# Kernel optimization log

Hardware: AMD Instinct MI355X
Metric: run time of the kernel (lower is better)

Reference implementation:

```python
import jax, jax.numpy as jnp
import numpy as np

B, N, C, P, K = 8, 65536, 96, 96, 512


def _ln(x, g, b, eps=1e-5):
    mu = x.mean(axis=-1, keepdims=True)
    var = ((x - mu) ** 2).mean(axis=-1, keepdims=True)
    return (x - mu) * jax.lax.rsqrt(var + eps) * g + b


def setup_inputs():
    key = jax.random.key(0)
    ks = jax.random.split(key, 8)
    inp = {
        "pts_feat": jax.random.normal(ks[0], (B, N, C), jnp.float32),
        "sp_idx": jax.random.randint(ks[1], (B, N), 0, K, jnp.int64),
        "all_xyz": jax.random.normal(ks[2], (B, N, 3), jnp.float32),
        # pts_proj1: Linear(3,P) -> LN -> ReLU -> Linear(P,P) -> LN
        "W1": jax.random.normal(ks[3], (3, P), jnp.float32) / np.sqrt(3.0),
        "b1": jnp.zeros((P,), jnp.float32),
        "g1": jnp.ones((P,), jnp.float32),
        "be1": jnp.zeros((P,), jnp.float32),
        "W2": jax.random.normal(ks[4], (P, P), jnp.float32) / np.sqrt(P),
        "b2": jnp.zeros((P,), jnp.float32),
        "g2": jnp.ones((P,), jnp.float32),
        "be2": jnp.zeros((P,), jnp.float32),
        # pts_proj2: Linear(2P,P) -> LN -> ReLU -> Linear(P,1,no bias) -> Sigmoid
        "W3": jax.random.normal(ks[5], (2 * P, P), jnp.float32) / np.sqrt(2.0 * P),
        "b3": jnp.zeros((P,), jnp.float32),
        "g3": jnp.ones((P,), jnp.float32),
        "be3": jnp.zeros((P,), jnp.float32),
        "W4": jax.random.normal(ks[6], (P, 1), jnp.float32) / np.sqrt(P),
        "num_sp": K,
    }
    return inp


def reference(pts_feat, sp_idx, all_xyz, W1, b1, g1, be1, W2, b2, g2, be2,
              W3, b3, g3, be3, W4, num_sp):
    Bx, Nx, Cx = pts_feat.shape
    S = Bx * num_sp  # total superpoints across batch (uniform K per batch)
    idx = (sp_idx + jnp.arange(Bx, dtype=sp_idx.dtype)[:, None] * num_sp).reshape(-1)
    xyz = all_xyz.reshape(-1, 3)
    feat = pts_feat.reshape(-1, Cx)

    # scatter_norm: unit-sphere normalize per segment
    mn = jax.ops.segment_min(xyz, idx, num_segments=S)
    mx = jax.ops.segment_max(xyz, idx, num_segments=S)
    cnt = jax.ops.segment_sum(jnp.ones((xyz.shape[0],), xyz.dtype), idx, num_segments=S)
    cnt_c = jnp.maximum(cnt, 1.0)
    center = jax.ops.segment_sum(xyz, idx, num_segments=S) / cnt_c[:, None]
    diam = (mx - mn).max(axis=1)
    pts = (xyz - center[idx]) / (diam[idx][:, None] + 0.01)

    # pts_proj1
    h = _ln(pts @ W1 + b1, g1, be1)
    h = jax.nn.relu(h)
    h = _ln(h @ W2 + b2, g2, be2)

    seg = jax.ops.segment_max(h, idx, num_segments=S)  # (S, P)
    cat = jnp.concatenate([h, seg[idx]], axis=-1)      # (B*N, 2P)

    # pts_proj2
    z = _ln(cat @ W3 + b3, g3, be3)
    z = jax.nn.relu(z)
    w = jax.nn.sigmoid(z @ W4) * 2.0                   # (B*N, 1)

    sp_feat = jax.ops.segment_sum(feat * w, idx, num_segments=S) / cnt_c[:, None] + seg
    return sp_feat.reshape(Bx, num_sp, Cx), w.reshape(Bx, Nx, 1)
```

## Files before the change

### kernel.cpp

```cpp
#include <hip/hip_runtime.h>
#include <cstdint>

#define MM 524288
#define NSEG 4096

#define WS_SCNT   0u
#define WS_CURSOR 4096u
#define WS_OFFS   8192u
#define WS_M1     12288u
#define WS_CENTER 12304u
#define WS_DIAM   24592u
#define WS_SEGF   28688u
#define WS_ZSEG   421904u
#define WS_SORTED 815120u
#define WS_SEG16  1339408u
#define WS_WSRT   1601552u
#define WS_H8     2125840u
#define WS_END    (WS_H8 + 25165824u)

typedef __attribute__((ext_vector_type(8))) short short8;
typedef __attribute__((ext_vector_type(4))) float f32x4;

#define WPAD 104

__device__ __forceinline__ unsigned bfr(float x) {
    unsigned u = __float_as_uint(x);
    return (u + 0x7FFFu + ((u >> 16) & 1u)) >> 16;
}
__device__ __forceinline__ float bf2f(unsigned v) {
    return __uint_as_float(v << 16);
}
union U4S8 { uint4 u; short8 s; };

__global__ void __launch_bounds__(256) k0_init(unsigned* __restrict__ ws)
{
    unsigned i = blockIdx.x * 256u + threadIdx.x;
    if (i < 8192u) ws[i] = 0u;
}

__global__ void __launch_bounds__(256) k1_count(
    const int* __restrict__ spidx, unsigned* __restrict__ scnt)
{
    __shared__ unsigned lcnt[512];
    int tid = threadIdx.x;
    for (int j = tid; j < 512; j += 256) lcnt[j] = 0u;
    __syncthreads();
    int base = blockIdx.x * 4096;
    #pragma unroll 4
    for (int it = 0; it < 16; ++it) {
        int p = base + it*256 + tid;
        atomicAdd(&lcnt[spidx[p]], 1u);
    }
    __syncthreads();
    int b = blockIdx.x >> 4;
    for (int j = tid; j < 512; j += 256)
        atomicAdd(&scnt[(b << 9) + j], lcnt[j]);
}

__global__ void __launch_bounds__(1024) k2_scan(
    const unsigned* __restrict__ scnt, unsigned* __restrict__ offs,
    const float* __restrict__ W1, const float* __restrict__ b1, float* __restrict__ m1)
{
    __shared__ unsigned sh[1024];
    int t = threadIdx.x;
    unsigned c0 = scnt[t*4+0], c1 = scnt[t*4+1], c2 = scnt[t*4+2], c3 = scnt[t*4+3];
    unsigned tot = c0 + c1 + c2 + c3;
    sh[t] = tot;
    __syncthreads();
    for (int d = 1; d < 1024; d <<= 1) {
        unsigned v = (t >= d) ? sh[t-d] : 0u;
        __syncthreads();
        sh[t] += v;
        __syncthreads();
    }
    unsigned excl = sh[t] - tot;
    offs[t*4+0] = excl;
    offs[t*4+1] = excl + c0;
    offs[t*4+2] = excl + c0 + c1;
    offs[t*4+3] = excl + c0 + c1 + c2;

    if (t == 0) {
        float Sa=0,Sb=0,Sc=0,Sd=0,Saa=0,Sbb=0,Scc=0,Sdd=0,Sab=0,Sac=0,Sad=0,Sbc=0,Sbd=0,Scd=0;
        #pragma unroll 8
        for (int j = 0; j < 96; ++j) {
            float A = W1[j], B2 = W1[96+j], C2 = W1[192+j], D = b1[j];
            Sa+=A; Sb+=B2; Sc+=C2; Sd+=D;
            Saa=fmaf(A,A,Saa); Sbb=fmaf(B2,B2,Sbb); Scc=fmaf(C2,C2,Scc); Sdd=fmaf(D,D,Sdd);
            Sab=fmaf(A,B2,Sab); Sac=fmaf(A,C2,Sac); Sad=fmaf(A,D,Sad);
            Sbc=fmaf(B2,C2,Sbc); Sbd=fmaf(B2,D,Sbd); Scd=fmaf(C2,D,Scd);
        }
        const float inv = 1.f/96.f;
        float Am=Sa*inv, Bm=Sb*inv, Cm=Sc*inv, Dm=Sd*inv;
        m1[0]=Am; m1[1]=Bm; m1[2]=Cm; m1[3]=Dm;
        m1[4]=Saa*inv-Am*Am; m1[5]=Sbb*inv-Bm*Bm; m1[6]=Scc*inv-Cm*Cm; m1[7]=Sdd*inv-Dm*Dm;
        m1[8]=Sab*inv-Am*Bm; m1[9]=Sac*inv-Am*Cm; m1[10]=Sad*inv-Am*Dm;
        m1[11]=Sbc*inv-Bm*Cm; m1[12]=Sbd*inv-Bm*Dm; m1[13]=Scd*inv-Cm*Dm;
    }
}

__global__ void __launch_bounds__(256) k3_scatter(
    const int* __restrict__ spidx, const unsigned* __restrict__ offs,
    unsigned* __restrict__ cursor, unsigned* __restrict__ sorted,
    unsigned short* __restrict__ seg16)
{
    __shared__ unsigned lcnt[512];
    __shared__ unsigned gbase[512];
    __shared__ unsigned short rank16[4096];
    int tid = threadIdx.x;
    for (int j = tid; j < 512; j += 256) lcnt[j] = 0u;
    __syncthreads();
    int base = blockIdx.x * 4096;
    #pragma unroll 4
    for (int it = 0; it < 16; ++it) {
        int p = base + it*256 + tid;
        unsigned r = atomicAdd(&lcnt[spidx[p]], 1u);
        rank16[it*256 + tid] = (unsigned short)r;
    }
    __syncthreads();
    int b = blockIdx.x >> 4;
    for (int j = tid; j < 512; j += 256)
        gbase[j] = atomicAdd(&cursor[(b << 9) + j], lcnt[j]);
    __syncthreads();
    #pragma unroll 4
    for (int it = 0; it < 16; ++it) {
        int p = base + it*256 + tid;
        int sl = spidx[p];
        int s = (b << 9) + sl;
        unsigned pos = offs[s] + gbase[sl] + (unsigned)rank16[it*256 + tid];
        sorted[pos] = (unsigned)p;
        seg16[pos] = (unsigned short)s;
    }
}

__global__ void __launch_bounds__(128) k3b_stats(
    const float* __restrict__ xyz, const unsigned* __restrict__ sorted,
    const unsigned* __restrict__ offs, const unsigned* __restrict__ scnt,
    float* __restrict__ center, float* __restrict__ diam)
{
    int s = blockIdx.x, tid = threadIdx.x;
    unsigned cnt = scnt[s], off = offs[s];
    float mnx=INFINITY, mny=INFINITY, mnz=INFINITY;
    float mxx=-INFINITY, mxy=-INFINITY, mxz=-INFINITY;
    float smx=0.f, smy=0.f, smz=0.f;
    for (unsigned r = tid; r < cnt; r += 128) {
        unsigned p = sorted[off + r];
        float x = xyz[3*p], y = xyz[3*p+1], z = xyz[3*p+2];
        mnx = fminf(mnx, x); mny = fminf(mny, y); mnz = fminf(mnz, z);
        mxx = fmaxf(mxx, x); mxy = fmaxf(mxy, y); mxz = fmaxf(mxz, z);
        smx += x; smy += y; smz += z;
    }
    #pragma unroll
    for (int m = 1; m < 64; m <<= 1) {
        mnx = fminf(mnx, __shfl_xor(mnx, m)); mny = fminf(mny, __shfl_xor(mny, m));
        mnz = fminf(mnz, __shfl_xor(mnz, m));
        mxx = fmaxf(mxx, __shfl_xor(mxx, m)); mxy = fmaxf(mxy, __shfl_xor(mxy, m));
        mxz = fmaxf(mxz, __shfl_xor(mxz, m));
        smx += __shfl_xor(smx, m); smy += __shfl_xor(smy, m); smz += __shfl_xor(smz, m);
    }
    __shared__ float cw[2][9];
    if ((tid & 63) == 0) {
        int w = tid >> 6;
        cw[w][0]=mnx; cw[w][1]=mny; cw[w][2]=mnz;
        cw[w][3]=mxx; cw[w][4]=mxy; cw[w][5]=mxz;
        cw[w][6]=smx; cw[w][7]=smy; cw[w][8]=smz;
    }
    __syncthreads();
    if (tid == 0) {
        float a0=fminf(cw[0][0],cw[1][0]), a1=fminf(cw[0][1],cw[1][1]), a2=fminf(cw[0][2],cw[1][2]);
        float b0=fmaxf(cw[0][3],cw[1][3]), b1=fmaxf(cw[0][4],cw[1][4]), b2=fmaxf(cw[0][5],cw[1][5]);
        float s0=cw[0][6]+cw[1][6], s1=cw[0][7]+cw[1][7], s2=cw[0][8]+cw[1][8];
        float cc = fmaxf((float)cnt, 1.f);
        center[s*3+0] = s0/cc; center[s*3+1] = s1/cc; center[s*3+2] = s2/cc;
        diam[s] = fmaxf(fmaxf(b0-a0, b1-a1), b2-a2);
    }
}

__global__ void __launch_bounds__(256) kTA(
    const float* __restrict__ xyz,
    const unsigned* __restrict__ sorted,
    const unsigned short* __restrict__ seg16,
    const float* __restrict__ center, const float* __restrict__ diam,
    const float* __restrict__ W1, const float* __restrict__ b1,
    const float* __restrict__ g1, const float* __restrict__ be1,
    const float* __restrict__ m1,
    const float* __restrict__ W2, const float* __restrict__ b2,
    const float* __restrict__ g2, const float* __restrict__ be2,
    uint4* __restrict__ h8)
{
    __shared__ unsigned short wT[96*WPAD];
    __shared__ float pw[96*6];
    __shared__ float prm[3*96];
    int tid = threadIdx.x;
    #pragma unroll 4
    for (int it = 0; it < 36; ++it) {
        int e = it*256 + tid;
        int i = e / 96, j = e - i*96;
        wT[j*WPAD + i] = (unsigned short)bfr(W2[e]);
    }
    if (tid < 96) {
        pw[tid*6+0] = W1[tid]; pw[tid*6+1] = W1[96+tid]; pw[tid*6+2] = W1[192+tid];
        pw[tid*6+3] = b1[tid]; pw[tid*6+4] = g1[tid];    pw[tid*6+5] = be1[tid];
        prm[tid] = b2[tid]; prm[96+tid] = g2[tid]; prm[192+tid] = be2[tid];
    }
    __syncthreads();

    float mc[14];
    #pragma unroll
    for (int k = 0; k < 14; ++k) mc[k] = m1[k];

    int lane = tid & 63, w = tid >> 6;
    int pcol = lane & 15, g = lane >> 4;
    size_t slot0 = (size_t)blockIdx.x * 256 + w*64 + pcol;

    #pragma unroll 1
    for (int t = 0; t < 4; ++t) {
        size_t slot = slot0 + (size_t)t * 16;
        unsigned p = sorted[slot];
        int s = seg16[slot];
        float dinv = 1.f / (diam[s] + 0.01f);
        float px = (xyz[3*p+0] - center[3*s+0]) * dinv;
        float py = (xyz[3*p+1] - center[3*s+1]) * dinv;
        float pz = (xyz[3*p+2] - center[3*s+2]) * dinv;

        float mu = fmaf(px, mc[0], fmaf(py, mc[1], fmaf(pz, mc[2], mc[3])));
        float var = fmaf(px*px, mc[4], fmaf(py*py, mc[5], fmaf(pz*pz, mc[6], mc[7])));
        var = fmaf(2.f*px*py, mc[8],  var);
        var = fmaf(2.f*px*pz, mc[9],  var);
        var = fmaf(2.f*px,    mc[10], var);
        var = fmaf(2.f*py*pz, mc[11], var);
        var = fmaf(2.f*py,    mc[12], var);
        var = fmaf(2.f*pz,    mc[13], var);
        float rs = rsqrtf(var + 1e-5f);

        U4S8 bu[3];
        #pragma unroll
        for (int ks = 0; ks < 3; ++ks) {
            unsigned vv[4];
            #pragma unroll
            for (int e2 = 0; e2 < 4; ++e2) {
                int i0 = ks*32 + g*8 + e2*2;
                const float* r0 = &pw[i0*6];
                float ta = fmaf(px, r0[0], fmaf(py, r0[1], fmaf(pz, r0[2], r0[3])));
                ta = fmaxf(fmaf((ta - mu) * rs, r0[4], r0[5]), 0.f);
                const float* r1 = &pw[(i0+1)*6];
                float tb = fmaf(px, r1[0], fmaf(py, r1[1], fmaf(pz, r1[2], r1[3])));
                tb = fmaxf(fmaf((tb - mu) * rs, r1[4], r1[5]), 0.f);
                vv[e2] = bfr(ta) | (bfr(tb) << 16);
            }
            bu[ks].u.x = vv[0]; bu[ks].u.y = vv[1]; bu[ks].u.z = vv[2]; bu[ks].u.w = vv[3];
        }

        f32x4 acc[6];
        #pragma unroll
        for (int nt = 0; nt < 6; ++nt) acc[nt] = (f32x4){0.f,0.f,0.f,0.f};

        #pragma unroll
        for (int ks = 0; ks < 3; ++ks) {
            #pragma unroll
            for (int nt = 0; nt < 6; ++nt) {
                const short8 aF = *(const short8*)&wT[(nt*16 + pcol)*WPAD + ks*32 + g*8];
                acc[nt] = __builtin_amdgcn_mfma_f32_16x16x32_bf16(aF, bu[ks].s, acc[nt], 0, 0, 0);
            }
        }

        float sum = 0.f, sq = 0.f;
        #pragma unroll
        for (int nt = 0; nt < 6; ++nt) {
            f32x4 bv = *(const f32x4*)&prm[nt*16 + g*4];
            #pragma unroll
            for (int r = 0; r < 4; ++r) {
                float v = acc[nt][r] + bv[r];
                acc[nt][r] = v;
                sum += v;
                sq = fmaf(v, v, sq);
            }
        }
        sum += __shfl_xor(sum, 16); sum += __shfl_xor(sum, 32);
        sq  += __shfl_xor(sq, 16);  sq  += __shfl_xor(sq, 32);
        float muh = sum * (1.f/96.f);
        float rsh = rsqrtf(sq * (1.f/96.f) - muh*muh + 1e-5f);

        #pragma unroll
        for (int nt = 0; nt < 6; ++nt) {
            f32x4 gv  = *(const f32x4*)&prm[96  + nt*16 + g*4];
            f32x4 bev = *(const f32x4*)&prm[192 + nt*16 + g*4];
            float o0 = fmaf((acc[nt][0]-muh)*rsh, gv[0], bev[0]);
            float o1 = fmaf((acc[nt][1]-muh)*rsh, gv[1], bev[1]);
            float o2 = fmaf((acc[nt][2]-muh)*rsh, gv[2], bev[2]);
            float o3 = fmaf((acc[nt][3]-muh)*rsh, gv[3], bev[3]);
            uint2 st;
            st.x = bfr(o0) | (bfr(o1) << 16);
            st.y = bfr(o2) | (bfr(o3) << 16);
            int j0 = nt*16 + g*4;
            size_t q = (size_t)(nt*2 + (g >> 1));
            *(uint2*)((char*)h8 + (q*MM + slot)*16 + (size_t)(j0 & 7)*2) = st;
        }
    }
}

__global__ void __launch_bounds__(192) kB_seg(
    const uint4* __restrict__ h8,
    const unsigned* __restrict__ offs, const unsigned* __restrict__ scnt,
    const float* __restrict__ W3, const float* __restrict__ b3,
    float* __restrict__ segf, float* __restrict__ zseg)
{
    __shared__ uint4 st[16][13];
    __shared__ float lseg[96];
    int s = blockIdx.x, tid = threadIdx.x;
    unsigned cnt = scnt[s], off = offs[s];
    int r = tid & 15, q = tid >> 4;
    float mx = -INFINITY;
    for (unsigned base = 0; base < cnt; base += 16) {
        uint4 v = make_uint4(0xFF80FF80u, 0xFF80FF80u, 0xFF80FF80u, 0xFF80FF80u);
        if (q < 12 && base + (unsigned)r < cnt)
            v = h8[(size_t)q * MM + off + base + r];
        if (q < 12) st[r][q] = v;
        __syncthreads();
        if (tid < 96) {
            int qj = tid >> 3, ej = tid & 7;
            #pragma unroll
            for (int rr = 0; rr < 16; ++rr) {
                const unsigned short* hp = (const unsigned short*)&st[rr][qj];
                mx = fmaxf(mx, bf2f(hp[ej]));
            }
        }
        __syncthreads();
    }
    if (tid < 96) { segf[(size_t)s*96 + tid] = mx; lseg[tid] = mx; }
    __syncthreads();
    if (tid < 96) {
        float acc = b3[tid];
        #pragma unroll 4
        for (int i = 0; i < 96; ++i)
            acc = fmaf(lseg[i], W3[(size_t)(96+i)*96 + tid], acc);
        zseg[(size_t)s*96 + tid] = acc;
    }
}

__global__ void __launch_bounds__(256) kC_mfma(
    const uint4* __restrict__ h8, const float* __restrict__ zseg,
    const unsigned short* __restrict__ seg16, const unsigned* __restrict__ sorted,
    const float* __restrict__ W3, const float* __restrict__ g3,
    const float* __restrict__ be3, const float* __restrict__ W4,
    float* __restrict__ w_nat, float* __restrict__ w_srt)
{
    __shared__ unsigned short wT[96*WPAD];
    __shared__ float prm[3*96];
    int tid = threadIdx.x;
    #pragma unroll 4
    for (int it = 0; it < 36; ++it) {
        int e = it*256 + tid;
        int i = e / 96, j = e - i*96;
        wT[j*WPAD + i] = (unsigned short)bfr(W3[e]);
    }
    if (tid < 96) { prm[tid] = g3[tid]; prm[96+tid] = be3[tid]; prm[192+tid] = W4[tid]; }
    __syncthreads();

    int lane = tid & 63, w = tid >> 6;
    int pcol = lane & 15, g = lane >> 4;
    size_t slot0 = (size_t)blockIdx.x * 256 + w*64 + pcol;

    #pragma unroll 1
    for (int t = 0; t < 4; ++t) {
        size_t slot = slot0 + (size_t)t * 16;
        U4S8 bu[3];
        #pragma unroll
        for (int ks = 0; ks < 3; ++ks)
            bu[ks].u = h8[(size_t)(ks*4+g) * MM + slot];

        f32x4 acc[6];
        #pragma unroll
        for (int nt = 0; nt < 6; ++nt) acc[nt] = (f32x4){0.f,0.f,0.f,0.f};

        #pragma unroll
        for (int ks = 0; ks < 3; ++ks) {
            #pragma unroll
            for (int nt = 0; nt < 6; ++nt) {
                const short8 aF = *(const short8*)&wT[(nt*16 + pcol)*WPAD + ks*32 + g*8];
                acc[nt] = __builtin_amdgcn_mfma_f32_16x16x32_bf16(aF, bu[ks].s, acc[nt], 0, 0, 0);
            }
        }

        int s = seg16[slot];
        float sum = 0.f, sq = 0.f;
        #pragma unroll
        for (int nt = 0; nt < 6; ++nt) {
            f32x4 zs = *(const f32x4*)&zseg[(size_t)s*96 + nt*16 + g*4];
            #pragma unroll
            for (int r = 0; r < 4; ++r) {
                float v = acc[nt][r] + zs[r];
                acc[nt][r] = v;
                sum += v;
                sq = fmaf(v, v, sq);
            }
        }
        sum += __shfl_xor(sum, 16); sum += __shfl_xor(sum, 32);
        sq  += __shfl_xor(sq, 16);  sq  += __shfl_xor(sq, 32);
        float mu = sum * (1.f/96.f);
        float rs = rsqrtf(sq * (1.f/96.f) - mu*mu + 1e-5f);

        float tt = 0.f;
        #pragma unroll
        for (int nt = 0; nt < 6; ++nt) {
            f32x4 gv  = *(const f32x4*)&prm[nt*16 + g*4];
            f32x4 bev = *(const f32x4*)&prm[96 + nt*16 + g*4];
            f32x4 w4v = *(const f32x4*)&prm[192 + nt*16 + g*4];
            #pragma unroll
            for (int r = 0; r < 4; ++r) {
                float v = fmaxf(fmaf((acc[nt][r]-mu)*rs, gv[r], bev[r]), 0.f);
                tt = fmaf(v, w4v[r], tt);
            }
        }
        tt += __shfl_xor(tt, 16); tt += __shfl_xor(tt, 32);
        if (lane < 16) {
            float wv = 2.f / (1.f + expf(-tt));
            w_srt[slot] = wv;
            w_nat[sorted[slot]] = wv;
        }
    }
}

__global__ void __launch_bounds__(128) kD_pool(
    const float* __restrict__ feat, const float* __restrict__ w_srt,
    const unsigned* __restrict__ sorted, const unsigned* __restrict__ offs,
    const unsigned* __restrict__ scnt, const float* __restrict__ segf,
    float* __restrict__ sp_out)
{
    int s = blockIdx.x;
    int c = threadIdx.x;
    unsigned cnt = scnt[s], off = offs[s];
    float acc = 0.f;
    unsigned r = 0;
    for (; r + 4 <= cnt; r += 4) {
        unsigned p0 = sorted[off+r],   p1 = sorted[off+r+1];
        unsigned p2 = sorted[off+r+2], p3 = sorted[off+r+3];
        float w0 = w_srt[off+r], w1 = w_srt[off+r+1], w2 = w_srt[off+r+2], w3 = w_srt[off+r+3];
        if (c < 96) {
            acc = fmaf(feat[(size_t)p0*96 + c], w0, acc);
            acc = fmaf(feat[(size_t)p1*96 + c], w1, acc);
            acc = fmaf(feat[(size_t)p2*96 + c], w2, acc);
            acc = fmaf(feat[(size_t)p3*96 + c], w3, acc);
        }
    }
    for (; r < cnt; ++r) {
        unsigned p0 = sorted[off+r];
        float w0 = w_srt[off+r];
        if (c < 96) acc = fmaf(feat[(size_t)p0*96 + c], w0, acc);
    }
    if (c < 96) {
        float cc = fmaxf((float)cnt, 1.f);
        sp_out[(size_t)s*96 + c] = acc / cc + segf[(size_t)s*96 + c];
    }
}

extern "C" void kernel_launch(void* const* d_in, const int* in_sizes, int n_in,
                              void* d_out, int out_size, void* d_ws, size_t ws_size,
                              hipStream_t stream)
{
    const float* pts_feat = (const float*)d_in[0];
    const int*   sp_idx   = (const int*)d_in[1];
    const float* xyz      = (const float*)d_in[2];
    const float* W1  = (const float*)d_in[3];
    const float* b1  = (const float*)d_in[4];
    const float* g1  = (const float*)d_in[5];
    const float* be1 = (const float*)d_in[6];
    const float* W2  = (const float*)d_in[7];
    const float* b2  = (const float*)d_in[8];
    const float* g2  = (const float*)d_in[9];
    const float* be2 = (const float*)d_in[10];
    const float* W3  = (const float*)d_in[11];
    const float* b3  = (const float*)d_in[12];
    const float* g3  = (const float*)d_in[13];
    const float* be3 = (const float*)d_in[14];
    const float* W4  = (const float*)d_in[15];

    float* out = (float*)d_out;
    float* sp_out = out;
    float* w_out  = out + (size_t)NSEG * 96;

    if (ws_size < (size_t)WS_END * 4u) return;

    unsigned* ws32   = (unsigned*)d_ws;
    unsigned* scnt   = ws32 + WS_SCNT;
    unsigned* cursor = ws32 + WS_CURSOR;
    unsigned* offs   = ws32 + WS_OFFS;
    float*    m1     = (float*)(ws32 + WS_M1);
    float*    center = (float*)(ws32 + WS_CENTER);
    float*    diam   = (float*)(ws32 + WS_DIAM);
    float*    segf   = (float*)(ws32 + WS_SEGF);
    float*    zseg   = (float*)(ws32 + WS_ZSEG);
    unsigned* sorted = ws32 + WS_SORTED;
    unsigned short* seg16 = (unsigned short*)(ws32 + WS_SEG16);
    float*    w_srt  = (float*)(ws32 + WS_WSRT);
    uint4*    h8     = (uint4*)(ws32 + WS_H8);

    k0_init<<<32, 256, 0, stream>>>(ws32);
    k1_count<<<MM/4096, 256, 0, stream>>>(sp_idx, scnt);
    k2_scan<<<1, 1024, 0, stream>>>(scnt, offs, W1, b1, m1);
    k3_scatter<<<MM/4096, 256, 0, stream>>>(sp_idx, offs, cursor, sorted, seg16);
    k3b_stats<<<NSEG, 128, 0, stream>>>(xyz, sorted, offs, scnt, center, diam);
    kTA<<<MM/256, 256, 0, stream>>>(xyz, sorted, seg16, center, diam,
        W1, b1, g1, be1, m1, W2, b2, g2, be2, h8);
    kB_seg<<<NSEG, 192, 0, stream>>>(h8, offs, scnt, W3, b3, segf, zseg);
    kC_mfma<<<MM/256, 256, 0, stream>>>(h8, zseg, seg16, sorted, W3, g3, be3, W4,
        w_out, w_srt);
    kD_pool<<<NSEG, 128, 0, stream>>>(pts_feat, w_srt, sorted, offs, scnt, segf, sp_out);
}
```

Before: 265.0 us.

## Pad segments to 16-slot windows and fuse segment max into projection kernel

Each segment's slot range is padded to a multiple of 16, so every 16-row MFMA tile in kTA belongs to exactly one segment. kTA now computes a per-window max of h with shuffles and writes it out, and the new kZ_seg reduces only those window maxima instead of rereading the full h8 buffer. k3b_stats also writes the normalized points in sorted order, removing per-point center and diameter gathers from kTA, and kD_pool's loop is unrolled by 8. The cost is extra padded slots, a larger workspace init, sentinel handling for invalid slots, and extra shuffle work in kTA.

```diff
diff --git a/kernel.cpp b/kernel.cpp
--- a/kernel.cpp
+++ b/kernel.cpp
@@ -3,20 +3,22 @@
 
 #define MM 524288
 #define NSEG 4096
+#define NSLOT 585728u
+#define NWIN 36608u
 
 #define WS_SCNT   0u
 #define WS_CURSOR 4096u
-#define WS_OFFS   8192u
+#define WS_OFFSP  8192u
 #define WS_M1     12288u
-#define WS_CENTER 12304u
-#define WS_DIAM   24592u
-#define WS_SEGF   28688u
-#define WS_ZSEG   421904u
-#define WS_SORTED 815120u
-#define WS_SEG16  1339408u
-#define WS_WSRT   1601552u
-#define WS_H8     2125840u
-#define WS_END    (WS_H8 + 25165824u)
+#define WS_SEGF   12304u
+#define WS_ZSEG   405520u
+#define WS_SORTED 798736u
+#define WS_SEG16  1384464u
+#define WS_WSRT   1677328u
+#define WS_PTS    2263056u
+#define WS_WMAX   4020240u
+#define WS_H8     5777424u
+#define WS_END    33892368u
 
 typedef __attribute__((ext_vector_type(8))) short short8;
 typedef __attribute__((ext_vector_type(4))) float f32x4;
@@ -36,6 +38,8 @@
 {
     unsigned i = blockIdx.x * 256u + threadIdx.x;
     if (i < 8192u) ws[i] = 0u;
+    else if (i < 8192u + NSLOT) ws[WS_SORTED + (i - 8192u)] = 0xFFFFFFFFu;
+    else ws[WS_SEG16 + (i - 8192u - NSLOT)] = 0u;
 }
 
 __global__ void __launch_bounds__(256) k1_count(
@@ -58,12 +62,13 @@
 }
 
 __global__ void __launch_bounds__(1024) k2_scan(
-    const unsigned* __restrict__ scnt, unsigned* __restrict__ offs,
+    const unsigned* __restrict__ scnt, unsigned* __restrict__ offsP,
     const float* __restrict__ W1, const float* __restrict__ b1, float* __restrict__ m1)
 {
     __shared__ unsigned sh[1024];
     int t = threadIdx.x;
-    unsigned c0 = scnt[t*4+0], c1 = scnt[t*4+1], c2 = scnt[t*4+2], c3 = scnt[t*4+3];
+    unsigned c0 = (scnt[t*4+0] + 15u) & ~15u, c1 = (scnt[t*4+1] + 15u) & ~15u;
+    unsigned c2 = (scnt[t*4+2] + 15u) & ~15u, c3 = (scnt[t*4+3] + 15u) & ~15u;
     unsigned tot = c0 + c1 + c2 + c3;
     sh[t] = tot;
     __syncthreads();
@@ -74,10 +79,10 @@
         __syncthreads();
     }
     unsigned excl = sh[t] - tot;
-    offs[t*4+0] = excl;
-    offs[t*4+1] = excl + c0;
-    offs[t*4+2] = excl + c0 + c1;
-    offs[t*4+3] = excl + c0 + c1 + c2;
+    offsP[t*4+0] = excl;
+    offsP[t*4+1] = excl + c0;
+    offsP[t*4+2] = excl + c0 + c1;
+    offsP[t*4+3] = excl + c0 + c1 + c2;
 
     if (t == 0) {
         float Sa=0,Sb=0,Sc=0,Sd=0,Saa=0,Sbb=0,Scc=0,Sdd=0,Sab=0,Sac=0,Sad=0,Sbc=0,Sbd=0,Scd=0;
@@ -99,7 +104,7 @@
 }
 
 __global__ void __launch_bounds__(256) k3_scatter(
-    const int* __restrict__ spidx, const unsigned* __restrict__ offs,
+    const int* __restrict__ spidx, const unsigned* __restrict__ offsP,
     unsigned* __restrict__ cursor, unsigned* __restrict__ sorted,
     unsigned short* __restrict__ seg16)
 {
@@ -126,7 +131,7 @@
         int p = base + it*256 + tid;
         int sl = spidx[p];
         int s = (b << 9) + sl;
-        unsigned pos = offs[s] + gbase[sl] + (unsigned)rank16[it*256 + tid];
+        unsigned pos = offsP[s] + gbase[sl] + (unsigned)rank16[it*256 + tid];
         sorted[pos] = (unsigned)p;
         seg16[pos] = (unsigned short)s;
     }
@@ -134,11 +139,11 @@
 
 __global__ void __launch_bounds__(128) k3b_stats(
     const float* __restrict__ xyz, const unsigned* __restrict__ sorted,
-    const unsigned* __restrict__ offs, const unsigned* __restrict__ scnt,
-    float* __restrict__ center, float* __restrict__ diam)
+    const unsigned* __restrict__ offsP, const unsigned* __restrict__ scnt,
+    float* __restrict__ pts)
 {
     int s = blockIdx.x, tid = threadIdx.x;
-    unsigned cnt = scnt[s], off = offs[s];
+    unsigned cnt = scnt[s], off = offsP[s];
     float mnx=INFINITY, mny=INFINITY, mnz=INFINITY;
     float mxx=-INFINITY, mxy=-INFINITY, mxz=-INFINITY;
     float smx=0.f, smy=0.f, smz=0.f;
@@ -158,6 +163,7 @@
         smx += __shfl_xor(smx, m); smy += __shfl_xor(smy, m); smz += __shfl_xor(smz, m);
     }
     __shared__ float cw[2][9];
+    __shared__ float cd[4];
     if ((tid & 63) == 0) {
         int w = tid >> 6;
         cw[w][0]=mnx; cw[w][1]=mny; cw[w][2]=mnz;
@@ -170,26 +176,103 @@
         float b0=fmaxf(cw[0][3],cw[1][3]), b1=fmaxf(cw[0][4],cw[1][4]), b2=fmaxf(cw[0][5],cw[1][5]);
         float s0=cw[0][6]+cw[1][6], s1=cw[0][7]+cw[1][7], s2=cw[0][8]+cw[1][8];
         float cc = fmaxf((float)cnt, 1.f);
-        center[s*3+0] = s0/cc; center[s*3+1] = s1/cc; center[s*3+2] = s2/cc;
-        diam[s] = fmaxf(fmaxf(b0-a0, b1-a1), b2-a2);
+        float dm = fmaxf(fmaxf(b0-a0, b1-a1), b2-a2);
+        cd[0] = s0/cc; cd[1] = s1/cc; cd[2] = s2/cc;
+        cd[3] = 1.f / (dm + 0.01f);
+    }
+    __syncthreads();
+    float cx = cd[0], cy = cd[1], cz = cd[2], dinv = cd[3];
+    for (unsigned r = tid; r < cnt; r += 128) {
+        unsigned p = sorted[off + r];
+        size_t o = (size_t)(off + r) * 3;
+        pts[o+0] = (xyz[3*p+0] - cx) * dinv;
+        pts[o+1] = (xyz[3*p+1] - cy) * dinv;
+        pts[o+2] = (xyz[3*p+2] - cz) * dinv;
+    }
+}
+
+__device__ __forceinline__ void compute_h(
+    float px, float py, float pz, const float* mc,
+    const unsigned short* wT, const float* pw, const float* prm2,
+    int pcol, int g, f32x4 acc[6])
+{
+    float mu = fmaf(px, mc[0], fmaf(py, mc[1], fmaf(pz, mc[2], mc[3])));
+    float var = fmaf(px*px, mc[4], fmaf(py*py, mc[5], fmaf(pz*pz, mc[6], mc[7])));
+    var = fmaf(2.f*px*py, mc[8],  var);
+    var = fmaf(2.f*px*pz, mc[9],  var);
+    var = fmaf(2.f*px,    mc[10], var);
+    var = fmaf(2.f*py*pz, mc[11], var);
+    var = fmaf(2.f*py,    mc[12], var);
+    var = fmaf(2.f*pz,    mc[13], var);
+    float rs = rsqrtf(var + 1e-5f);
+
+    U4S8 bu[3];
+    #pragma unroll
+    for (int ks = 0; ks < 3; ++ks) {
+        unsigned vv[4];
+        #pragma unroll
+        for (int e2 = 0; e2 < 4; ++e2) {
+            int i0 = ks*32 + g*8 + e2*2;
+            const float* r0 = &pw[i0*6];
+            float ta = fmaf(px, r0[0], fmaf(py, r0[1], fmaf(pz, r0[2], r0[3])));
+            ta = fmaxf(fmaf((ta - mu) * rs, r0[4], r0[5]), 0.f);
+            const float* r1 = &pw[(i0+1)*6];
+            float tb = fmaf(px, r1[0], fmaf(py, r1[1], fmaf(pz, r1[2], r1[3])));
+            tb = fmaxf(fmaf((tb - mu) * rs, r1[4], r1[5]), 0.f);
+            vv[e2] = bfr(ta) | (bfr(tb) << 16);
+        }
+        bu[ks].u.x = vv[0]; bu[ks].u.y = vv[1]; bu[ks].u.z = vv[2]; bu[ks].u.w = vv[3];
+    }
+
+    #pragma unroll
+    for (int nt = 0; nt < 6; ++nt) acc[nt] = (f32x4){0.f,0.f,0.f,0.f};
+    #pragma unroll
+    for (int ks = 0; ks < 3; ++ks) {
+        #pragma unroll
+        for (int nt = 0; nt < 6; ++nt) {
+            const short8 aF = *(const short8*)&wT[(nt*16 + pcol)*WPAD + ks*32 + g*8];
+            acc[nt] = __builtin_amdgcn_mfma_f32_16x16x32_bf16(aF, bu[ks].s, acc[nt], 0, 0, 0);
+        }
+    }
+
+    float sum = 0.f, sq = 0.f;
+    #pragma unroll
+    for (int nt = 0; nt < 6; ++nt) {
+        f32x4 bv = *(const f32x4*)&prm2[nt*16 + g*4];
+        #pragma unroll
+        for (int r = 0; r < 4; ++r) {
+            float v = acc[nt][r] + bv[r];
+            acc[nt][r] = v;
+            sum += v;
+            sq = fmaf(v, v, sq);
+        }
+    }
+    sum += __shfl_xor(sum, 16); sum += __shfl_xor(sum, 32);
+    sq  += __shfl_xor(sq, 16);  sq  += __shfl_xor(sq, 32);
+    float muh = sum * (1.f/96.f);
+    float rsh = rsqrtf(sq * (1.f/96.f) - muh*muh + 1e-5f);
+    #pragma unroll
+    for (int nt = 0; nt < 6; ++nt) {
+        f32x4 gv  = *(const f32x4*)&prm2[96  + nt*16 + g*4];
+        f32x4 bev = *(const f32x4*)&prm2[192 + nt*16 + g*4];
+        #pragma unroll
+        for (int r = 0; r < 4; ++r)
+            acc[nt][r] = fmaf((acc[nt][r]-muh)*rsh, gv[r], bev[r]);
     }
 }
 
 __global__ void __launch_bounds__(256) kTA(
-    const float* __restrict__ xyz,
-    const unsigned* __restrict__ sorted,
-    const unsigned short* __restrict__ seg16,
-    const float* __restrict__ center, const float* __restrict__ diam,
+    const float* __restrict__ pts, const unsigned* __restrict__ sorted,
     const float* __restrict__ W1, const float* __restrict__ b1,
     const float* __restrict__ g1, const float* __restrict__ be1,
     const float* __restrict__ m1,
     const float* __restrict__ W2, const float* __restrict__ b2,
     const float* __restrict__ g2, const float* __restrict__ be2,
-    uint4* __restrict__ h8)
+    uint4* __restrict__ h8, unsigned short* __restrict__ wmax16)
 {
     __shared__ unsigned short wT[96*WPAD];
     __shared__ float pw[96*6];
-    __shared__ float prm[3*96];
+    __shared__ float prm2[3*96];
     int tid = threadIdx.x;
     #pragma unroll 4
     for (int it = 0; it < 36; ++it) {
@@ -200,7 +283,7 @@
     if (tid < 96) {
         pw[tid*6+0] = W1[tid]; pw[tid*6+1] = W1[96+tid]; pw[tid*6+2] = W1[192+tid];
         pw[tid*6+3] = b1[tid]; pw[tid*6+4] = g1[tid];    pw[tid*6+5] = be1[tid];
-        prm[tid] = b2[tid]; prm[96+tid] = g2[tid]; prm[192+tid] = be2[tid];
+        prm2[tid] = b2[tid]; prm2[96+tid] = g2[tid]; prm2[192+tid] = be2[tid];
     }
     __syncthreads();
 
@@ -216,117 +299,68 @@
     for (int t = 0; t < 4; ++t) {
         size_t slot = slot0 + (size_t)t * 16;
         unsigned p = sorted[slot];
-        int s = seg16[slot];
-        float dinv = 1.f / (diam[s] + 0.01f);
-        float px = (xyz[3*p+0] - center[3*s+0]) * dinv;
-        float py = (xyz[3*p+1] - center[3*s+1]) * dinv;
-        float pz = (xyz[3*p+2] - center[3*s+2]) * dinv;
-
-        float mu = fmaf(px, mc[0], fmaf(py, mc[1], fmaf(pz, mc[2], mc[3])));
-        float var = fmaf(px*px, mc[4], fmaf(py*py, mc[5], fmaf(pz*pz, mc[6], mc[7])));
-        var = fmaf(2.f*px*py, mc[8],  var);
-        var = fmaf(2.f*px*pz, mc[9],  var);
-        var = fmaf(2.f*px,    mc[10], var);
-        var = fmaf(2.f*py*pz, mc[11], var);
-        var = fmaf(2.f*py,    mc[12], var);
-        var = fmaf(2.f*pz,    mc[13], var);
-        float rs = rsqrtf(var + 1e-5f);
-
-        U4S8 bu[3];
-        #pragma unroll
-        for (int ks = 0; ks < 3; ++ks) {
-            unsigned vv[4];
-            #pragma unroll
-            for (int e2 = 0; e2 < 4; ++e2) {
-                int i0 = ks*32 + g*8 + e2*2;
-                const float* r0 = &pw[i0*6];
-                float ta = fmaf(px, r0[0], fmaf(py, r0[1], fmaf(pz, r0[2], r0[3])));
-                ta = fmaxf(fmaf((ta - mu) * rs, r0[4], r0[5]), 0.f);
-                const float* r1 = &pw[(i0+1)*6];
-                float tb = fmaf(px, r1[0], fmaf(py, r1[1], fmaf(pz, r1[2], r1[3])));
-                tb = fmaxf(fmaf((tb - mu) * rs, r1[4], r1[5]), 0.f);
-                vv[e2] = bfr(ta) | (bfr(tb) << 16);
-            }
-            bu[ks].u.x = vv[0]; bu[ks].u.y = vv[1]; bu[ks].u.z = vv[2]; bu[ks].u.w = vv[3];
-        }
+        bool valid = (p != 0xFFFFFFFFu);
+        float px = pts[slot*3+0], py = pts[slot*3+1], pz = pts[slot*3+2];
 
         f32x4 acc[6];
-        #pragma unroll
-        for (int nt = 0; nt < 6; ++nt) acc[nt] = (f32x4){0.f,0.f,0.f,0.f};
-
-        #pragma unroll
-        for (int ks = 0; ks < 3; ++ks) {
-            #pragma unroll
-            for (int nt = 0; nt < 6; ++nt) {
-                const short8 aF = *(const short8*)&wT[(nt*16 + pcol)*WPAD + ks*32 + g*8];
-                acc[nt] = __builtin_amdgcn_mfma_f32_16x16x32_bf16(aF, bu[ks].s, acc[nt], 0, 0, 0);
-            }
-        }
-
-        float sum = 0.f, sq = 0.f;
+        compute_h(px, py, pz, mc, wT, pw, prm2, pcol, g, acc);
+
         #pragma unroll
         for (int nt = 0; nt < 6; ++nt) {
-            f32x4 bv = *(const f32x4*)&prm[nt*16 + g*4];
-            #pragma unroll
-            for (int r = 0; r < 4; ++r) {
-                float v = acc[nt][r] + bv[r];
-                acc[nt][r] = v;
-                sum += v;
-                sq = fmaf(v, v, sq);
-            }
-        }
-        sum += __shfl_xor(sum, 16); sum += __shfl_xor(sum, 32);
-        sq  += __shfl_xor(sq, 16);  sq  += __shfl_xor(sq, 32);
-        float muh = sum * (1.f/96.f);
-        float rsh = rsqrtf(sq * (1.f/96.f) - muh*muh + 1e-5f);
-
-        #pragma unroll
-        for (int nt = 0; nt < 6; ++nt) {
-            f32x4 gv  = *(const f32x4*)&prm[96  + nt*16 + g*4];
-            f32x4 bev = *(const f32x4*)&prm[192 + nt*16 + g*4];
-            float o0 = fmaf((acc[nt][0]-muh)*rsh, gv[0], bev[0]);
-            float o1 = fmaf((acc[nt][1]-muh)*rsh, gv[1], bev[1]);
-            float o2 = fmaf((acc[nt][2]-muh)*rsh, gv[2], bev[2]);
-            float o3 = fmaf((acc[nt][3]-muh)*rsh, gv[3], bev[3]);
             uint2 st;
-            st.x = bfr(o0) | (bfr(o1) << 16);
-            st.y = bfr(o2) | (bfr(o3) << 16);
+            st.x = bfr(acc[nt][0]) | (bfr(acc[nt][1]) << 16);
+            st.y = bfr(acc[nt][2]) | (bfr(acc[nt][3]) << 16);
             int j0 = nt*16 + g*4;
             size_t q = (size_t)(nt*2 + (g >> 1));
-            *(uint2*)((char*)h8 + (q*MM + slot)*16 + (size_t)(j0 & 7)*2) = st;
-        }
-    }
-}
-
-__global__ void __launch_bounds__(192) kB_seg(
-    const uint4* __restrict__ h8,
-    const unsigned* __restrict__ offs, const unsigned* __restrict__ scnt,
+            *(uint2*)((char*)h8 + (q*NSLOT + slot)*16 + (size_t)(j0 & 7)*2) = st;
+        }
+
+        if (!valid) {
+            #pragma unroll
+            for (int nt = 0; nt < 6; ++nt)
+                #pragma unroll
+                for (int r = 0; r < 4; ++r) acc[nt][r] = -INFINITY;
+        }
+        #pragma unroll
+        for (int m = 1; m < 16; m <<= 1) {
+            #pragma unroll
+            for (int nt = 0; nt < 6; ++nt) {
+                #pragma unroll
+                for (int r = 0; r < 4; ++r)
+                    acc[nt][r] = fmaxf(acc[nt][r], __shfl_xor(acc[nt][r], m));
+            }
+        }
+        if (pcol == 0) {
+            size_t wbase = (slot >> 4) * 96;
+            #pragma unroll
+            for (int nt = 0; nt < 6; ++nt) {
+                uint2 st;
+                st.x = bfr(acc[nt][0]) | (bfr(acc[nt][1]) << 16);
+                st.y = bfr(acc[nt][2]) | (bfr(acc[nt][3]) << 16);
+                *(uint2*)&wmax16[wbase + nt*16 + g*4] = st;
+            }
+        }
+    }
+}
+
+__global__ void __launch_bounds__(128) kZ_seg(
+    const unsigned short* __restrict__ wmax16,
+    const unsigned* __restrict__ offsP, const unsigned* __restrict__ scnt,
     const float* __restrict__ W3, const float* __restrict__ b3,
     float* __restrict__ segf, float* __restrict__ zseg)
 {
-    __shared__ uint4 st[16][13];
     __shared__ float lseg[96];
     int s = blockIdx.x, tid = threadIdx.x;
-    unsigned cnt = scnt[s], off = offs[s];
-    int r = tid & 15, q = tid >> 4;
-    float mx = -INFINITY;
-    for (unsigned base = 0; base < cnt; base += 16) {
-        uint4 v = make_uint4(0xFF80FF80u, 0xFF80FF80u, 0xFF80FF80u, 0xFF80FF80u);
-        if (q < 12 && base + (unsigned)r < cnt)
-            v = h8[(size_t)q * MM + off + base + r];
-        if (q < 12) st[r][q] = v;
-        __syncthreads();
-        if (tid < 96) {
-            int qj = tid >> 3, ej = tid & 7;
-            #pragma unroll
-            for (int rr = 0; rr < 16; ++rr) {
-                const unsigned short* hp = (const unsigned short*)&st[rr][qj];
-                mx = fmaxf(mx, bf2f(hp[ej]));
-            }
-        }
-        __syncthreads();
-    }
-    if (tid < 96) { segf[(size_t)s*96 + tid] = mx; lseg[tid] = mx; }
+    unsigned cnt = scnt[s];
+    unsigned win0 = offsP[s] >> 4;
+    unsigned nwin = (cnt + 15u) >> 4;
+    if (tid < 96) {
+        float mx = -INFINITY;
+        for (unsigned w = 0; w < nwin; ++w)
+            mx = fmaxf(mx, bf2f(wmax16[(size_t)(win0 + w)*96 + tid]));
+        segf[(size_t)s*96 + tid] = mx;
+        lseg[tid] = mx;
+    }
     __syncthreads();
     if (tid < 96) {
         float acc = b3[tid];
@@ -366,7 +400,7 @@
         U4S8 bu[3];
         #pragma unroll
         for (int ks = 0; ks < 3; ++ks)
-            bu[ks].u = h8[(size_t)(ks*4+g) * MM + slot];
+            bu[ks].u = h8[(size_t)(ks*4+g) * NSLOT + slot];
 
         f32x4 acc[6];
         #pragma unroll
@@ -414,37 +448,40 @@
         tt += __shfl_xor(tt, 16); tt += __shfl_xor(tt, 32);
         if (lane < 16) {
             float wv = 2.f / (1.f + expf(-tt));
+            unsigned p = sorted[slot];
             w_srt[slot] = wv;
-            w_nat[sorted[slot]] = wv;
+            if (p != 0xFFFFFFFFu) w_nat[p] = wv;
         }
     }
 }
 
 __global__ void __launch_bounds__(128) kD_pool(
     const float* __restrict__ feat, const float* __restrict__ w_srt,
-    const unsigned* __restrict__ sorted, const unsigned* __restrict__ offs,
+    const unsigned* __restrict__ sorted, const unsigned* __restrict__ offsP,
     const unsigned* __restrict__ scnt, const float* __restrict__ segf,
     float* __restrict__ sp_out)
 {
     int s = blockIdx.x;
     int c = threadIdx.x;
-    unsigned cnt = scnt[s], off = offs[s];
+    unsigned cnt = scnt[s], off = offsP[s];
     float acc = 0.f;
     unsigned r = 0;
-    for (; r + 4 <= cnt; r += 4) {
-        unsigned p0 = sorted[off+r],   p1 = sorted[off+r+1];
-        unsigned p2 = sorted[off+r+2], p3 = sorted[off+r+3];
-        float w0 = w_srt[off+r], w1 = w_srt[off+r+1], w2 = w_srt[off+r+2], w3 = w_srt[off+r+3];
+    for (; r + 8 <= cnt; r += 8) {
+        unsigned pp[8]; float ww[8];
+        #pragma unroll
+        for (int k = 0; k < 8; ++k) {
+            pp[k] = sorted[off + r + k];
+            ww[k] = w_srt[off + r + k];
+        }
         if (c < 96) {
-            acc = fmaf(feat[(size_t)p0*96 + c], w0, acc);
-            acc = fmaf(feat[(size_t)p1*96 + c], w1, acc);
-            acc = fmaf(feat[(size_t)p2*96 + c], w2, acc);
-            acc = fmaf(feat[(size_t)p3*96 + c], w3, acc);
+            #pragma unroll
+            for (int k = 0; k < 8; ++k)
+                acc = fmaf(feat[(size_t)pp[k]*96 + c], ww[k], acc);
         }
     }
     for (; r < cnt; ++r) {
-        unsigned p0 = sorted[off+r];
-        float w0 = w_srt[off+r];
+        unsigned p0 = sorted[off + r];
+        float w0 = w_srt[off + r];
         if (c < 96) acc = fmaf(feat[(size_t)p0*96 + c], w0, acc);
     }
     if (c < 96) {
@@ -483,26 +520,26 @@
     unsigned* ws32   = (unsigned*)d_ws;
     unsigned* scnt   = ws32 + WS_SCNT;
     unsigned* cursor = ws32 + WS_CURSOR;
-    unsigned* offs   = ws32 + WS_OFFS;
+    unsigned* offsP  = ws32 + WS_OFFSP;
     float*    m1     = (float*)(ws32 + WS_M1);
-    float*    center = (float*)(ws32 + WS_CENTER);
-    float*    diam   = (float*)(ws32 + WS_DIAM);
     float*    segf   = (float*)(ws32 + WS_SEGF);
     float*    zseg   = (float*)(ws32 + WS_ZSEG);
     unsigned* sorted = ws32 + WS_SORTED;
     unsigned short* seg16 = (unsigned short*)(ws32 + WS_SEG16);
     float*    w_srt  = (float*)(ws32 + WS_WSRT);
+    float*    pts    = (float*)(ws32 + WS_PTS);
+    unsigned short* wmax16 = (unsigned short*)(ws32 + WS_WMAX);
     uint4*    h8     = (uint4*)(ws32 + WS_H8);
 
-    k0_init<<<32, 256, 0, stream>>>(ws32);
+    k0_init<<<3464, 256, 0, stream>>>(ws32);
     k1_count<<<MM/4096, 256, 0, stream>>>(sp_idx, scnt);
-    k2_scan<<<1, 1024, 0, stream>>>(scnt, offs, W1, b1, m1);
-    k3_scatter<<<MM/4096, 256, 0, stream>>>(sp_idx, offs, cursor, sorted, seg16);
-    k3b_stats<<<NSEG, 128, 0, stream>>>(xyz, sorted, offs, scnt, center, diam);
-    kTA<<<MM/256, 256, 0, stream>>>(xyz, sorted, seg16, center, diam,
-        W1, b1, g1, be1, m1, W2, b2, g2, be2, h8);
-    kB_seg<<<NSEG, 192, 0, stream>>>(h8, offs, scnt, W3, b3, segf, zseg);
-    kC_mfma<<<MM/256, 256, 0, stream>>>(h8, zseg, seg16, sorted, W3, g3, be3, W4,
+    k2_scan<<<1, 1024, 0, stream>>>(scnt, offsP, W1, b1, m1);
+    k3_scatter<<<MM/4096, 256, 0, stream>>>(sp_idx, offsP, cursor, sorted, seg16);
+    k3b_stats<<<NSEG, 128, 0, stream>>>(xyz, sorted, offsP, scnt, pts);
+    kTA<<<NSLOT/256, 256, 0, stream>>>(pts, sorted, W1, b1, g1, be1, m1,
+        W2, b2, g2, be2, h8, wmax16);
+    kZ_seg<<<NSEG, 128, 0, stream>>>(wmax16, offsP, scnt, W3, b3, segf, zseg);
+    kC_mfma<<<NSLOT/256, 256, 0, stream>>>(h8, zseg, seg16, sorted, W3, g3, be3, W4,
         w_out, w_srt);
-    kD_pool<<<NSEG, 128, 0, stream>>>(pts_feat, w_srt, sorted, offs, scnt, segf, sp_out);
-}
+    kD_pool<<<NSEG, 128, 0, stream>>>(pts_feat, w_srt, sorted, offsP, scnt, segf, sp_out);
+}
```

Measured after the change: 345.5 us. +30.4%, slower.

## Split segment max into window-max pass plus segment combine; prefetch and tweak kernels

Applied to the files above, without the earlier changes.

The per-segment max over h moves from one block per segment, which looped serially over its rows through shared memory, into two kernels. A fully parallel pass first computes a max for each 16-slot window, and a second kernel combines those window maxima with the partial edge slots of each segment. Other changes: kC_mfma prefetches the next tile's h8 operands one iteration ahead, kTA interleaves the layer-1 compute with the MFMAs and uses padded vector LDS loads, and kD_pool unrolls its gather by 8. The cost is an extra launch and workspace buffer, plus more register pressure from the prefetch.

```diff
diff --git a/kernel.cpp b/kernel.cpp
--- a/kernel.cpp
+++ b/kernel.cpp
@@ -3,6 +3,7 @@
 
 #define MM 524288
 #define NSEG 4096
+#define NWIN2 32768u
 
 #define WS_SCNT   0u
 #define WS_CURSOR 4096u
@@ -16,7 +17,8 @@
 #define WS_SEG16  1339408u
 #define WS_WSRT   1601552u
 #define WS_H8     2125840u
-#define WS_END    (WS_H8 + 25165824u)
+#define WS_WMAX   27291664u
+#define WS_END    28864528u
 
 typedef __attribute__((ext_vector_type(8))) short short8;
 typedef __attribute__((ext_vector_type(4))) float f32x4;
@@ -188,8 +190,9 @@
     uint4* __restrict__ h8)
 {
     __shared__ unsigned short wT[96*WPAD];
-    __shared__ float pw[96*6];
+    __shared__ float pw8[96*8];
     __shared__ float prm[3*96];
+    __shared__ float mcl[14];
     int tid = threadIdx.x;
     #pragma unroll 4
     for (int it = 0; it < 36; ++it) {
@@ -198,19 +201,18 @@
         wT[j*WPAD + i] = (unsigned short)bfr(W2[e]);
     }
     if (tid < 96) {
-        pw[tid*6+0] = W1[tid]; pw[tid*6+1] = W1[96+tid]; pw[tid*6+2] = W1[192+tid];
-        pw[tid*6+3] = b1[tid]; pw[tid*6+4] = g1[tid];    pw[tid*6+5] = be1[tid];
+        pw8[tid*8+0] = W1[tid]; pw8[tid*8+1] = W1[96+tid]; pw8[tid*8+2] = W1[192+tid];
+        pw8[tid*8+3] = b1[tid]; pw8[tid*8+4] = g1[tid];    pw8[tid*8+5] = be1[tid];
+        pw8[tid*8+6] = 0.f;     pw8[tid*8+7] = 0.f;
         prm[tid] = b2[tid]; prm[96+tid] = g2[tid]; prm[192+tid] = be2[tid];
     }
-    __syncthreads();
-
-    float mc[14];
-    #pragma unroll
-    for (int k = 0; k < 14; ++k) mc[k] = m1[k];
+    if (tid < 14) mcl[tid] = m1[tid];
+    __syncthreads();
 
     int lane = tid & 63, w = tid >> 6;
     int pcol = lane & 15, g = lane >> 4;
     size_t slot0 = (size_t)blockIdx.x * 256 + w*64 + pcol;
+    const f32x4* pwv = (const f32x4*)pw8;
 
     #pragma unroll 1
     for (int t = 0; t < 4; ++t) {
@@ -222,44 +224,40 @@
         float py = (xyz[3*p+1] - center[3*s+1]) * dinv;
         float pz = (xyz[3*p+2] - center[3*s+2]) * dinv;
 
-        float mu = fmaf(px, mc[0], fmaf(py, mc[1], fmaf(pz, mc[2], mc[3])));
-        float var = fmaf(px*px, mc[4], fmaf(py*py, mc[5], fmaf(pz*pz, mc[6], mc[7])));
-        var = fmaf(2.f*px*py, mc[8],  var);
-        var = fmaf(2.f*px*pz, mc[9],  var);
-        var = fmaf(2.f*px,    mc[10], var);
-        var = fmaf(2.f*py*pz, mc[11], var);
-        var = fmaf(2.f*py,    mc[12], var);
-        var = fmaf(2.f*pz,    mc[13], var);
+        float mu = fmaf(px, mcl[0], fmaf(py, mcl[1], fmaf(pz, mcl[2], mcl[3])));
+        float var = fmaf(px*px, mcl[4], fmaf(py*py, mcl[5], fmaf(pz*pz, mcl[6], mcl[7])));
+        var = fmaf(2.f*px*py, mcl[8],  var);
+        var = fmaf(2.f*px*pz, mcl[9],  var);
+        var = fmaf(2.f*px,    mcl[10], var);
+        var = fmaf(2.f*py*pz, mcl[11], var);
+        var = fmaf(2.f*py,    mcl[12], var);
+        var = fmaf(2.f*pz,    mcl[13], var);
         float rs = rsqrtf(var + 1e-5f);
 
-        U4S8 bu[3];
+        f32x4 acc[6];
+        #pragma unroll
+        for (int nt = 0; nt < 6; ++nt) acc[nt] = (f32x4){0.f,0.f,0.f,0.f};
+
         #pragma unroll
         for (int ks = 0; ks < 3; ++ks) {
+            U4S8 bu;
             unsigned vv[4];
             #pragma unroll
             for (int e2 = 0; e2 < 4; ++e2) {
                 int i0 = ks*32 + g*8 + e2*2;
-                const float* r0 = &pw[i0*6];
-                float ta = fmaf(px, r0[0], fmaf(py, r0[1], fmaf(pz, r0[2], r0[3])));
-                ta = fmaxf(fmaf((ta - mu) * rs, r0[4], r0[5]), 0.f);
-                const float* r1 = &pw[(i0+1)*6];
-                float tb = fmaf(px, r1[0], fmaf(py, r1[1], fmaf(pz, r1[2], r1[3])));
-                tb = fmaxf(fmaf((tb - mu) * rs, r1[4], r1[5]), 0.f);
+                f32x4 lo0 = pwv[i0*2],     hi0 = pwv[i0*2+1];
+                f32x4 lo1 = pwv[(i0+1)*2], hi1 = pwv[(i0+1)*2+1];
+                float ta = fmaf(px, lo0[0], fmaf(py, lo0[1], fmaf(pz, lo0[2], lo0[3])));
+                ta = fmaxf(fmaf((ta - mu) * rs, hi0[0], hi0[1]), 0.f);
+                float tb = fmaf(px, lo1[0], fmaf(py, lo1[1], fmaf(pz, lo1[2], lo1[3])));
+                tb = fmaxf(fmaf((tb - mu) * rs, hi1[0], hi1[1]), 0.f);
                 vv[e2] = bfr(ta) | (bfr(tb) << 16);
             }
-            bu[ks].u.x = vv[0]; bu[ks].u.y = vv[1]; bu[ks].u.z = vv[2]; bu[ks].u.w = vv[3];
-        }
-
-        f32x4 acc[6];
-        #pragma unroll
-        for (int nt = 0; nt < 6; ++nt) acc[nt] = (f32x4){0.f,0.f,0.f,0.f};
-
-        #pragma unroll
-        for (int ks = 0; ks < 3; ++ks) {
+            bu.u.x = vv[0]; bu.u.y = vv[1]; bu.u.z = vv[2]; bu.u.w = vv[3];
             #pragma unroll
             for (int nt = 0; nt < 6; ++nt) {
                 const short8 aF = *(const short8*)&wT[(nt*16 + pcol)*WPAD + ks*32 + g*8];
-                acc[nt] = __builtin_amdgcn_mfma_f32_16x16x32_bf16(aF, bu[ks].s, acc[nt], 0, 0, 0);
+                acc[nt] = __builtin_amdgcn_mfma_f32_16x16x32_bf16(aF, bu.s, acc[nt], 0, 0, 0);
             }
         }
 
@@ -298,35 +296,62 @@
     }
 }
 
-__global__ void __launch_bounds__(192) kB_seg(
-    const uint4* __restrict__ h8,
+__global__ void __launch_bounds__(256) kW_winmax(
+    const unsigned* __restrict__ h8u32, unsigned* __restrict__ wmax32)
+{
+    unsigned gw = blockIdx.x * 4u + (threadIdx.x >> 6);
+    unsigned lane = threadIdx.x & 63u;
+    unsigned base = gw * 4u;
+    unsigned q = base >> 15;
+    unsigned win0 = base & 32767u;
+    size_t qoff = (size_t)q * MM * 4u;
+    #pragma unroll
+    for (int i = 0; i < 4; ++i) {
+        unsigned win = win0 + i;
+        unsigned v = h8u32[qoff + (size_t)win * 64u + lane];
+        float f0 = bf2f(v & 0xFFFFu);
+        float f1 = __uint_as_float(v & 0xFFFF0000u);
+        #pragma unroll
+        for (int m = 4; m < 64; m <<= 1) {
+            f0 = fmaxf(f0, __shfl_xor(f0, m));
+            f1 = fmaxf(f1, __shfl_xor(f1, m));
+        }
+        if (lane < 4) {
+            unsigned st = (__float_as_uint(f0) >> 16) | (__float_as_uint(f1) & 0xFFFF0000u);
+            wmax32[(size_t)win * 48u + q * 4u + lane] = st;
+        }
+    }
+}
+
+__global__ void __launch_bounds__(128) kZ_seg(
+    const unsigned short* __restrict__ wmax16,
+    const unsigned short* __restrict__ h8u16,
     const unsigned* __restrict__ offs, const unsigned* __restrict__ scnt,
     const float* __restrict__ W3, const float* __restrict__ b3,
     float* __restrict__ segf, float* __restrict__ zseg)
 {
-    __shared__ uint4 st[16][13];
     __shared__ float lseg[96];
     int s = blockIdx.x, tid = threadIdx.x;
     unsigned cnt = scnt[s], off = offs[s];
-    int r = tid & 15, q = tid >> 4;
-    float mx = -INFINITY;
-    for (unsigned base = 0; base < cnt; base += 16) {
-        uint4 v = make_uint4(0xFF80FF80u, 0xFF80FF80u, 0xFF80FF80u, 0xFF80FF80u);
-        if (q < 12 && base + (unsigned)r < cnt)
-            v = h8[(size_t)q * MM + off + base + r];
-        if (q < 12) st[r][q] = v;
-        __syncthreads();
-        if (tid < 96) {
-            int qj = tid >> 3, ej = tid & 7;
-            #pragma unroll
-            for (int rr = 0; rr < 16; ++rr) {
-                const unsigned short* hp = (const unsigned short*)&st[rr][qj];
-                mx = fmaxf(mx, bf2f(hp[ej]));
-            }
-        }
-        __syncthreads();
-    }
-    if (tid < 96) { segf[(size_t)s*96 + tid] = mx; lseg[tid] = mx; }
+    if (tid < 96) {
+        int q = tid >> 3, e = tid & 7;
+        size_t qstr = (size_t)q * MM * 8 + e;
+        unsigned a = off, b = off + cnt;
+        unsigned af = (a + 15u) & ~15u, bf = b & ~15u;
+        float mx = -INFINITY;
+        if (af < bf) {
+            for (unsigned wn = af >> 4; wn < (bf >> 4); ++wn)
+                mx = fmaxf(mx, bf2f(wmax16[(size_t)wn*96 + tid]));
+        }
+        unsigned h1 = min(af, b);
+        for (unsigned sl = a; sl < h1; ++sl)
+            mx = fmaxf(mx, bf2f(h8u16[qstr + (size_t)sl*8]));
+        unsigned t0 = max(bf, h1);
+        for (unsigned sl = t0; sl < b; ++sl)
+            mx = fmaxf(mx, bf2f(h8u16[qstr + (size_t)sl*8]));
+        segf[(size_t)s*96 + tid] = mx;
+        lseg[tid] = mx;
+    }
     __syncthreads();
     if (tid < 96) {
         float acc = b3[tid];
@@ -360,13 +385,22 @@
     int pcol = lane & 15, g = lane >> 4;
     size_t slot0 = (size_t)blockIdx.x * 256 + w*64 + pcol;
 
+    uint4 B0 = h8[(size_t)(0*4+g) * MM + slot0];
+    uint4 B1 = h8[(size_t)(1*4+g) * MM + slot0];
+    uint4 B2q = h8[(size_t)(2*4+g) * MM + slot0];
+
     #pragma unroll 1
     for (int t = 0; t < 4; ++t) {
         size_t slot = slot0 + (size_t)t * 16;
-        U4S8 bu[3];
-        #pragma unroll
-        for (int ks = 0; ks < 3; ++ks)
-            bu[ks].u = h8[(size_t)(ks*4+g) * MM + slot];
+        uint4 C0 = B0, C1 = B1, C2 = B2q;
+        if (t < 3) {
+            size_t sn = slot + 16;
+            C0 = h8[(size_t)(0*4+g) * MM + sn];
+            C1 = h8[(size_t)(1*4+g) * MM + sn];
+            C2 = h8[(size_t)(2*4+g) * MM + sn];
+        }
+        U4S8 u0, u1, u2; u0.u = B0; u1.u = B1; u2.u = B2q;
+        short8 bB[3] = { u0.s, u1.s, u2.s };
 
         f32x4 acc[6];
         #pragma unroll
@@ -377,7 +411,7 @@
             #pragma unroll
             for (int nt = 0; nt < 6; ++nt) {
                 const short8 aF = *(const short8*)&wT[(nt*16 + pcol)*WPAD + ks*32 + g*8];
-                acc[nt] = __builtin_amdgcn_mfma_f32_16x16x32_bf16(aF, bu[ks].s, acc[nt], 0, 0, 0);
+                acc[nt] = __builtin_amdgcn_mfma_f32_16x16x32_bf16(aF, bB[ks], acc[nt], 0, 0, 0);
             }
         }
 
@@ -417,6 +451,7 @@
             w_srt[slot] = wv;
             w_nat[sorted[slot]] = wv;
         }
+        B0 = C0; B1 = C1; B2q = C2;
     }
 }
 
@@ -431,20 +466,22 @@
     unsigned cnt = scnt[s], off = offs[s];
     float acc = 0.f;
     unsigned r = 0;
-    for (; r + 4 <= cnt; r += 4) {
-        unsigned p0 = sorted[off+r],   p1 = sorted[off+r+1];
-        unsigned p2 = sorted[off+r+2], p3 = sorted[off+r+3];
-        float w0 = w_srt[off+r], w1 = w_srt[off+r+1], w2 = w_srt[off+r+2], w3 = w_srt[off+r+3];
+    for (; r + 8 <= cnt; r += 8) {
+        unsigned pp[8]; float ww[8];
+        #pragma unroll
+        for (int k = 0; k < 8; ++k) {
+            pp[k] = sorted[off + r + k];
+            ww[k] = w_srt[off + r + k];
+        }
         if (c < 96) {
-            acc = fmaf(feat[(size_t)p0*96 + c], w0, acc);
-            acc = fmaf(feat[(size_t)p1*96 + c], w1, acc);
-            acc = fmaf(feat[(size_t)p2*96 + c], w2, acc);
-            acc = fmaf(feat[(size_t)p3*96 + c], w3, acc);
+            #pragma unroll
+            for (int k = 0; k < 8; ++k)
+                acc = fmaf(feat[(size_t)pp[k]*96 + c], ww[k], acc);
         }
     }
     for (; r < cnt; ++r) {
-        unsigned p0 = sorted[off+r];
-        float w0 = w_srt[off+r];
+        unsigned p0 = sorted[off + r];
+        float w0 = w_srt[off + r];
         if (c < 96) acc = fmaf(feat[(size_t)p0*96 + c], w0, acc);
     }
     if (c < 96) {
@@ -493,6 +530,7 @@
     unsigned short* seg16 = (unsigned short*)(ws32 + WS_SEG16);
     float*    w_srt  = (float*)(ws32 + WS_WSRT);
     uint4*    h8     = (uint4*)(ws32 + WS_H8);
+    unsigned* wmax32 = ws32 + WS_WMAX;
 
     k0_init<<<32, 256, 0, stream>>>(ws32);
     k1_count<<<MM/4096, 256, 0, stream>>>(sp_idx, scnt);
@@ -501,7 +539,9 @@
     k3b_stats<<<NSEG, 128, 0, stream>>>(xyz, sorted, offs, scnt, center, diam);
     kTA<<<MM/256, 256, 0, stream>>>(xyz, sorted, seg16, center, diam,
         W1, b1, g1, be1, m1, W2, b2, g2, be2, h8);
-    kB_seg<<<NSEG, 192, 0, stream>>>(h8, offs, scnt, W3, b3, segf, zseg);
+    kW_winmax<<<(NWIN2*12u)/16u, 256, 0, stream>>>((const unsigned*)h8, wmax32);
+    kZ_seg<<<NSEG, 128, 0, stream>>>((const unsigned short*)wmax32,
+        (const unsigned short*)h8, offs, scnt, W3, b3, segf, zseg);
     kC_mfma<<<MM/256, 256, 0, stream>>>(h8, zseg, seg16, sorted, W3, g3, be3, W4,
         w_out, w_srt);
     kD_pool<<<NSEG, 128, 0, stream>>>(pts_feat, w_srt, sorted, offs, scnt, segf, sp_out);
```

Result: slower. 303.8 us (+14.7%).
